# Performance work log

Hardware: AMD Instinct MI355X
Metric: run time of the kernel (lower is better)

Reference implementation:

```python
import jax, jax.numpy as jnp
import numpy as np

B, C, H, W = 8, 256, 64, 64
NH = 4
HD = C // NH
EPS_LN = 1e-5
EPS_NORM = 1e-12


def ln2d(x, w, b):
    # LayerNorm over channel dim of NCHW, per spatial location
    m = jnp.mean(x, axis=1, keepdims=True)
    v = jnp.mean((x - m) ** 2, axis=1, keepdims=True)
    return (x - m) / jnp.sqrt(v + EPS_LN) * w[None, :, None, None] + b[None, :, None, None]


def l2norm(x):
    # F.normalize(x, dim=-1)
    n = jnp.sqrt(jnp.sum(x * x, axis=-1, keepdims=True))
    return x / jnp.maximum(n, EPS_NORM)


def setup_inputs() -> dict:
    key = jax.random.key(0)
    ks = jax.random.split(key, 12)
    s = 0.02
    return {
        "img_feat": jax.random.normal(ks[0], (B, C, H, W), jnp.float32),
        "aux0": jax.random.normal(ks[1], (B, C, H, W), jnp.float32),
        "aux1": jax.random.normal(ks[2], (B, C, H, W), jnp.float32),
        "q_ln_w": jnp.ones((C,), jnp.float32),
        "q_ln_b": jnp.zeros((C,), jnp.float32),
        "kv_ln_w": jnp.ones((C,), jnp.float32),
        "kv_ln_b": jnp.zeros((C,), jnp.float32),
        "Wq": jax.random.normal(ks[3], (C, C), jnp.float32) * s,
        "Wkv": jax.random.normal(ks[4], (2 * C, C), jnp.float32) * s,
        "Wo": jax.random.normal(ks[5], (C, C), jnp.float32) * s,
        "bo": jnp.zeros((C,), jnp.float32),
        "attn_scale": jnp.zeros((NH, 1, 1), jnp.float32),
        "mlp_ln_w": jnp.ones((C,), jnp.float32),
        "mlp_ln_b": jnp.zeros((C,), jnp.float32),
        "W1": jax.random.normal(ks[6], (C, C), jnp.float32) * s,
        "b1": jnp.zeros((C,), jnp.float32),
        "W2": jax.random.normal(ks[7], (C, C), jnp.float32) * s,
        "b2": jnp.zeros((C,), jnp.float32),
    }


def reference(img_feat, aux0, aux1, q_ln_w, q_ln_b, kv_ln_w, kv_ln_b,
              Wq, Wkv, Wo, bo, attn_scale, mlp_ln_w, mlp_ln_b, W1, b1, W2, b2):
    HWn = H * W
    # q branch
    q = ln2d(img_feat, q_ln_w, q_ln_b).reshape(B, C, HWn)
    q = jnp.einsum('oc,bcn->bon', Wq, q).reshape(B, NH, HD, HWn)
    # kv branch: cat aux feats along batch (2B)
    kv_in = jnp.concatenate([aux0, aux1], axis=0)
    kv = ln2d(kv_in, kv_ln_w, kv_ln_b).reshape(2 * B, C, HWn)
    kv = jnp.einsum('oc,bcn->bon', Wkv, kv).reshape(2 * B, 2, NH, HD, HWn)
    k, v = kv[:, 0], kv[:, 1]  # each (2B, nh, hd, hw)
    qn = l2norm(q)
    kn = l2norm(k)
    kt, kd = kn[:B], kn[B:]
    vt, vd = v[:B], v[B:]
    # transposed (cross-covariance) cosine attention: hd x hd score matrix
    tex_attn = jax.nn.softmax(jnp.einsum('bnch,bndh->bncd', qn, kt), axis=-1)
    dep_attn = jax.nn.softmax(jnp.einsum('bnch,bndh->bncd', qn, kd), axis=-1)
    tex_qkv = jnp.einsum('bncd,bndh->bnch', tex_attn, vt)
    dep_qkv = jnp.einsum('bncd,bndh->bnch', dep_attn, vd)
    gate = jax.nn.sigmoid(attn_scale)[None]  # (1, nh, 1, 1)
    qkv = gate * tex_qkv + (1.0 - gate) * dep_qkv  # (B, nh, hd, hw)
    qkv = qkv.reshape(B, C, HWn)
    o = jnp.einsum('oc,bcn->bon', Wo, qkv).reshape(B, C, H, W) + bo[None, :, None, None]
    x = img_feat + o
    # ConvMlp (norm_ffn): LayerNorm2d -> 1x1 conv -> GELU -> 1x1 conv
    y = ln2d(x, mlp_ln_w, mlp_ln_b).reshape(B, C, HWn)
    y = jnp.einsum('oc,bcn->bon', W1, y) + b1[None, :, None]
    y = jax.nn.gelu(y)
    y = jnp.einsum('oc,bcn->bon', W2, y) + b2[None, :, None]
    return x + y.reshape(B, C, H, W)
```

## Files before the change

kernel.cpp:

```cpp
#include <hip/hip_runtime.h>
#include <math.h>
#include <stdint.h>

#define B_   8
#define C_   256
#define N_   4096

typedef __bf16 bf16;
typedef __bf16 bf16x8 __attribute__((ext_vector_type(8)));
typedef __bf16 bf16x4 __attribute__((ext_vector_type(4)));
typedef float  f32x4  __attribute__((ext_vector_type(4)));

#define MFMA16(a, b, c) __builtin_amdgcn_mfma_f32_16x16x32_bf16((a), (b), (c), 0, 0, 0)

struct Ptrs { const void* p[18]; };

__device__ __forceinline__ f32x4 ld4(const void* p, long i, bool f32) {
    f32x4 r;
    if (f32) {
        r = *(const f32x4*)((const float*)p + i);
    } else {
        bf16x4 v = *(const bf16x4*)((const bf16*)p + i);
        r[0] = (float)v[0]; r[1] = (float)v[1]; r[2] = (float)v[2]; r[3] = (float)v[3];
    }
    return r;
}

__device__ __forceinline__ float wave_sum(float s) {
    #pragma unroll
    for (int off = 32; off; off >>= 1) s += __shfl_xor(s, off);
    return s;
}

__device__ __forceinline__ void gl_lds16(const bf16* g, bf16* l) {
    __builtin_amdgcn_global_load_lds(
        (const __attribute__((address_space(1))) void*)(uintptr_t)g,
        (__attribute__((address_space(3))) void*)(uintptr_t)l, 16, 0, 0);
}

__global__ __launch_bounds__(256) void prep_kernel(Ptrs a, bf16* __restrict__ wb,
                                                   float* __restrict__ Sbuf,
                                                   bf16* __restrict__ biasb) {
    bool f32 = ((const unsigned*)a.p[3])[0] == 0x3F800000u;
    int row = blockIdx.x * 4 + (threadIdx.x >> 6);
    int lane = threadIdx.x & 63;
    long c4 = lane * 4;
    if (row >= 1536) {
        if (row == 1539) {
            if (lane == 0) {
                f32x4 v = ld4(a.p[11], 0, f32);
                #pragma unroll
                for (int j = 0; j < 4; ++j) biasb[768 + j] = (bf16)v[j];
            }
        } else {
            const void* s = (row == 1536) ? a.p[10] : (row == 1537) ? a.p[15] : a.p[17];
            f32x4 v = ld4(s, c4, f32);
            bf16x4 o;
            #pragma unroll
            for (int j = 0; j < 4; ++j) o[j] = (bf16)v[j];
            *(bf16x4*)(biasb + (row - 1536) * 256 + c4) = o;
        }
        return;
    }
    const void *W, *lw = nullptr, *lb = nullptr;
    long wrow; bf16* dst; float *s1 = nullptr, *s2 = nullptr;
    if (row < 256)       { W = a.p[7];  lw = a.p[3];  lb = a.p[4];  wrow = row;        dst = wb + row * 256;                 s1 = Sbuf + row;          s2 = Sbuf + 256 + row; }
    else if (row < 768)  { W = a.p[8];  lw = a.p[5];  lb = a.p[6];  wrow = row - 256;  dst = wb + 65536 + wrow * 256;        s1 = Sbuf + 512 + wrow;   s2 = Sbuf + 1024 + wrow; }
    else if (row < 1024) { W = a.p[14]; lw = a.p[12]; lb = a.p[13]; wrow = row - 768;  dst = wb + 196608 + wrow * 256;       s1 = Sbuf + 1536 + wrow;  s2 = Sbuf + 1792 + wrow; }
    else if (row < 1280) { W = a.p[9];  wrow = row - 1024; dst = wb + 262144 + wrow * 256; }
    else                 { W = a.p[16]; wrow = row - 1280; dst = wb + 327680 + wrow * 256; }
    f32x4 W4 = ld4(W, wrow * 256 + c4, f32);
    f32x4 w4, b4;
    if (lw) { w4 = ld4(lw, c4, f32); b4 = ld4(lb, c4, f32); }
    else    { w4[0]=w4[1]=w4[2]=w4[3]=1.f; b4[0]=b4[1]=b4[2]=b4[3]=0.f; }
    bf16x4 o;
    float s1v = 0.f, s2v = 0.f;
    #pragma unroll
    for (int j = 0; j < 4; ++j) {
        float wp = W4[j] * w4[j];
        o[j] = (bf16)wp;
        s1v += wp;
        s2v += W4[j] * b4[j];
    }
    *(bf16x4*)(dst + c4) = o;
    if (s1) {
        s1v = wave_sum(s1v); s2v = wave_sum(s2v);
        if (lane == 0) { *s1 = s1v; *s2 = s2v; }
    }
}

__global__ __launch_bounds__(256) void transpose_kernel(Ptrs a, bf16* __restrict__ xT) {
    bool f32 = ((const unsigned*)a.p[3])[0] == 0x3F800000u;
    int gt = blockIdx.z;
    const void* src; int batch;
    if (gt < 8)       { src = a.p[0]; batch = gt; }
    else if (gt < 16) { src = a.p[1]; batch = gt - 8; }
    else              { src = a.p[2]; batch = gt - 16; }
    int c0 = blockIdx.y * 64, n0 = blockIdx.x * 64;
    int t = threadIdx.x;
    __shared__ bf16 T[64][72];
    int cl = t >> 4, n4 = (t & 15) * 4;
    #pragma unroll
    for (int i = 0; i < 4; ++i) {
        int c = i * 16 + cl;
        f32x4 v = ld4(src, ((long)batch * 256 + c0 + c) * 4096 + n0 + n4, f32);
        #pragma unroll
        for (int j = 0; j < 4; ++j) T[c][n4 + j] = (bf16)v[j];
    }
    __syncthreads();
    int c8 = (t & 7) * 8, nl = t >> 3;
    #pragma unroll
    for (int j = 0; j < 2; ++j) {
        int n = j * 32 + nl;
        bf16x8 o;
        #pragma unroll
        for (int jj = 0; jj < 8; ++jj) o[jj] = T[c8 + jj][n];
        *(bf16x8*)(xT + ((size_t)gt * 4096 + n0 + n) * 256 + c0 + c8) = o;
    }
}

__global__ __launch_bounds__(256) void statsT_kernel(const bf16* __restrict__ xT,
                                                     float2* __restrict__ st) {
    int row = blockIdx.x * 4 + (threadIdx.x >> 6);
    int lane = threadIdx.x & 63;
    bf16x4 v = *(const bf16x4*)(xT + (size_t)row * 256 + lane * 4);
    float s = 0.f, q = 0.f;
    #pragma unroll
    for (int j = 0; j < 4; ++j) { float f = (float)v[j]; s += f; q += f * f; }
    s = wave_sum(s); q = wave_sum(q);
    if (lane == 0) {
        float mean = s * (1.0f / 256.0f);
        float var  = q * (1.0f / 256.0f) - mean * mean;
        float2 o; o.x = mean; o.y = rsqrtf(var + 1e-5f);
        st[row] = o;
    }
}

__global__ __launch_bounds__(256, 2) void wgemm_kernel(const bf16* __restrict__ A,
                                                    const bf16* __restrict__ xT,
                                                    const float2* __restrict__ stats,
                                                    const float* __restrict__ S1,
                                                    const float* __restrict__ S2,
                                                    const bf16* __restrict__ bias,
                                                    const bf16* __restrict__ resT,
                                                    void* __restrict__ out,
                                                    bf16* __restrict__ vT,
                                                    const unsigned* __restrict__ probe,
                                                    int emode, int gelu) {
    int n0 = blockIdx.x * 128;
    int ot = blockIdx.y;
    int g  = blockIdx.z;
    int t = threadIdx.x, wv = t >> 6, lane = t & 63;
    int m16 = lane & 15, quad = lane >> 4;
    int wr = wv >> 1, wc = wv & 1;
    int rl = lane >> 3, slot = lane & 7;

    __shared__ bf16 As[2][128 * 64];
    __shared__ bf16 Bs[2][128 * 64];

    const bf16* Agbase = A + (size_t)ot * 128 * 256;
    const bf16* Bgbase = xT + ((size_t)g * 4096 + n0) * 256;

    auto stage = [&](int buf, int ks) {
        #pragma unroll
        for (int i = 0; i < 4; ++i) {
            int row = wv * 32 + i * 8 + rl;
            int koff = ks * 64 + ((slot ^ (row & 7)) << 3);
            bf16* ldsA = &As[buf][(wv * 32 + i * 8) * 64];
            bf16* ldsB = &Bs[buf][(wv * 32 + i * 8) * 64];
            gl_lds16(Agbase + (size_t)row * 256 + koff, ldsA);
            gl_lds16(Bgbase + (size_t)row * 256 + koff, ldsB);
        }
    };

    f32x4 acc[4][4];
    #pragma unroll
    for (int i = 0; i < 4; ++i)
        #pragma unroll
        for (int j = 0; j < 4; ++j) acc[i][j] = (f32x4){0.f, 0.f, 0.f, 0.f};

    auto compute = [&](int buf) {
        #pragma unroll
        for (int kf = 0; kf < 2; ++kf) {
            bf16x8 af[4], bv[4];
            #pragma unroll
            for (int mt = 0; mt < 4; ++mt) {
                int r = wr * 64 + mt * 16 + m16;
                af[mt] = *(const bf16x8*)&As[buf][r * 64 + (((kf * 4 + quad) ^ (r & 7)) << 3)];
            }
            #pragma unroll
            for (int nt = 0; nt < 4; ++nt) {
                int r = wc * 64 + nt * 16 + m16;
                bv[nt] = *(const bf16x8*)&Bs[buf][r * 64 + (((kf * 4 + quad) ^ (r & 7)) << 3)];
            }
            #pragma unroll
            for (int mt = 0; mt < 4; ++mt)
                #pragma unroll
                for (int nt = 0; nt < 4; ++nt)
                    acc[mt][nt] = MFMA16(af[mt], bv[nt], acc[mt][nt]);
        }
    };

    stage(0, 0);
    __syncthreads();
    #pragma unroll
    for (int ks = 0; ks < 4; ++ks) {
        if (ks < 3) stage((ks + 1) & 1, ks + 1);
        compute(ks & 1);
        __syncthreads();
    }

    int of32 = (emode == 3) ? (probe[0] == 0x3F800000u) : 0;

    #pragma unroll
    for (int mt = 0; mt < 4; ++mt) {
        int olb  = wr * 64 + mt * 16 + quad * 4;
        int orow = ot * 128 + olb;
        f32x4 s1v, s2v, bz;
        if (stats) { s1v = *(const f32x4*)(S1 + orow); s2v = *(const f32x4*)(S2 + orow); }
        if (bias) {
            bf16x4 bb = *(const bf16x4*)(bias + orow);
            #pragma unroll
            for (int r = 0; r < 4; ++r) bz[r] = (float)bb[r];
        }
        #pragma unroll
        for (int nt = 0; nt < 4; ++nt) {
            int n = n0 + wc * 64 + nt * 16 + m16;
            f32x4 v = acc[mt][nt];
            if (stats) {
                float2 st = stats[(size_t)g * N_ + n];
                float a1 = st.y, a2 = -st.y * st.x;
                #pragma unroll
                for (int r = 0; r < 4; ++r) v[r] = a1 * v[r] + a2 * s1v[r] + s2v[r];
            }
            if (bias) {
                #pragma unroll
                for (int r = 0; r < 4; ++r) v[r] += bz[r];
            }
            if (gelu) {
                #pragma unroll
                for (int r = 0; r < 4; ++r) {
                    float x = v[r];
                    float u = x + 0.044715f * x * x * x;
                    v[r] = 0.5f * x * (1.0f + tanhf(0.7978845608028654f * u));
                }
            }
            if (emode == 0) {
                if (vT == nullptr || orow < 256) {
                    bf16* o = (bf16*)out;
                    #pragma unroll
                    for (int r = 0; r < 4; ++r)
                        o[((size_t)(g * 256 + orow + r)) * N_ + n] = (bf16)v[r];
                } else {
                    int od = orow - 256;
                    int hh = od >> 6, d0 = od & 63;
                    bf16x4 tmp;
                    #pragma unroll
                    for (int r = 0; r < 4; ++r) tmp[r] = (bf16)v[r];
                    *(bf16x4*)(vT + (((size_t)(g * 4 + hh)) * N_ + n) * 64 + d0) = tmp;
                }
            } else if (emode == 2) {
                size_t idx = ((size_t)g * N_ + n) * 256 + orow;
                if (resT) {
                    bf16x4 rr = *(const bf16x4*)(resT + idx);
                    #pragma unroll
                    for (int r = 0; r < 4; ++r) v[r] += (float)rr[r];
                }
                bf16x4 tmp;
                #pragma unroll
                for (int r = 0; r < 4; ++r) tmp[r] = (bf16)v[r];
                *(bf16x4*)((bf16*)out + idx) = tmp;
            } else {
                bf16x4 rr = *(const bf16x4*)(resT + ((size_t)g * N_ + n) * 256 + orow);
                #pragma unroll
                for (int r = 0; r < 4; ++r) {
                    float val = v[r] + (float)rr[r];
                    size_t oi = ((size_t)(g * 256 + orow + r)) * N_ + n;
                    if (of32) ((float*)out)[oi] = val;
                    else      ((bf16*)out)[oi] = (bf16)val;
                }
            }
        }
    }
}

__global__ __launch_bounds__(256) void rownorm_kernel(const bf16* __restrict__ x,
                                                      float* __restrict__ invn) {
    size_t row = blockIdx.x;
    const bf16* p = x + (row << 12);
    int t = threadIdx.x;
    float s = 0.f;
    #pragma unroll
    for (int i = 0; i < 2; ++i) {
        bf16x8 v = *(const bf16x8*)(p + ((size_t)(i * 256 + t) << 3));
        #pragma unroll
        for (int j = 0; j < 8; ++j) { float f = (float)v[j]; s += f * f; }
    }
    #pragma unroll
    for (int off = 32; off > 0; off >>= 1) s += __shfl_down(s, off);
    __shared__ float ps[4];
    if ((t & 63) == 0) ps[t >> 6] = s;
    __syncthreads();
    if (t == 0) {
        float tot = ps[0] + ps[1] + ps[2] + ps[3];
        invn[row] = 1.0f / fmaxf(sqrtf(tot), 1e-12f);
    }
}

__global__ __launch_bounds__(256) void sgemm_kernel(const bf16* __restrict__ q,
                                                    const bf16* __restrict__ k,
                                                    float* __restrict__ Spart) {
    int bh = blockIdx.x, ks = blockIdx.y;
    int b = bh >> 2, h = bh & 3;
    int t = threadIdx.x, wv = t >> 6, lane = t & 63;
    int m16 = lane & 15, quad = lane >> 4;
    const bf16* qrow = q + (size_t)(b * 256 + h * 64 + wv * 16 + m16) * N_;
    const bf16* kt0  = k + (size_t)(b * 256 + h * 64) * N_;
    const bf16* kd0  = k + (size_t)((b + 8) * 256 + h * 64) * N_;

    f32x4 at[4], ad[4];
    #pragma unroll
    for (int i = 0; i < 4; ++i) { at[i] = (f32x4){0.f,0.f,0.f,0.f}; ad[i] = (f32x4){0.f,0.f,0.f,0.f}; }

    int nbeg = ks * 512;
    for (int n = nbeg; n < nbeg + 512; n += 32) {
        int ko = n + quad * 8;
        bf16x8 a = *(const bf16x8*)(qrow + ko);
        #pragma unroll
        for (int dt = 0; dt < 4; ++dt) {
            bf16x8 bt = *(const bf16x8*)(kt0 + (size_t)(dt * 16 + m16) * N_ + ko);
            at[dt] = MFMA16(a, bt, at[dt]);
            bf16x8 bd = *(const bf16x8*)(kd0 + (size_t)(dt * 16 + m16) * N_ + ko);
            ad[dt] = MFMA16(a, bd, ad[dt]);
        }
    }
    float* oT = Spart + (size_t)(ks * 32 + bh) * 4096;
    float* oD = Spart + (size_t)8 * 32 * 4096 + (size_t)(ks * 32 + bh) * 4096;
    #pragma unroll
    for (int dt = 0; dt < 4; ++dt)
        #pragma unroll
        for (int r = 0; r < 4; ++r) {
            int c = wv * 16 + quad * 4 + r, d = dt * 16 + m16;
            oT[c * 64 + d] = at[dt][r];
            oD[c * 64 + d] = ad[dt][r];
        }
}

__global__ __launch_bounds__(256) void softmax_kernel(const float* __restrict__ Spart,
                                                      const float* __restrict__ invnq,
                                                      const float* __restrict__ invnk,
                                                      const bf16* __restrict__ attn_scale,
                                                      bf16* __restrict__ Acat) {
    int bh = blockIdx.x;
    int h = bh & 3;
    int t = threadIdx.x, wv = t >> 6, lane = t & 63;
    float g = 1.0f / (1.0f + expf(-(float)attn_scale[h]));
    #pragma unroll
    for (int i = 0; i < 4; ++i) {
        int idx = blockIdx.y * 16 + wv * 4 + i;
        int stream = idx >> 6, c = idx & 63;
        const float* Sp = Spart + (size_t)stream * 8 * 32 * 4096 + (size_t)bh * 4096 + c * 64 + lane;
        float s = 0.f;
        #pragma unroll
        for (int ks = 0; ks < 8; ++ks) s += Sp[(size_t)ks * 32 * 4096];
        s *= invnq[bh * 64 + c] * invnk[(stream ? bh + 32 : bh) * 64 + lane];
        float mx = s;
        #pragma unroll
        for (int off = 32; off > 0; off >>= 1) mx = fmaxf(mx, __shfl_xor(mx, off));
        float e = expf(s - mx);
        float sum = e;
        #pragma unroll
        for (int off = 32; off > 0; off >>= 1) sum += __shfl_xor(sum, off);
        float a = e / sum * (stream == 0 ? g : 1.0f - g);
        Acat[(size_t)bh * 8192 + c * 128 + stream * 64 + lane] = (bf16)a;
    }
}

__global__ __launch_bounds__(256) void av_kernel(const bf16* __restrict__ Acat,
                                                 const bf16* __restrict__ vT,
                                                 bf16* __restrict__ qkvT) {
    int pt = blockIdx.x, h = blockIdx.y, b = blockIdx.z;
    int bh = b * 4 + h;
    int t = threadIdx.x, wv = t >> 6, lane = t & 63;
    int m16 = lane & 15, quad = lane >> 4;
    int p0 = pt * 64;

    const bf16* Arow = Acat + (size_t)bh * 8192 + (size_t)(wv * 16 + m16) * 128 + quad * 8;
    bf16x8 a[4];
    #pragma unroll
    for (int ds = 0; ds < 4; ++ds) a[ds] = *(const bf16x8*)(Arow + ds * 32);

    f32x4 acc[4];
    #pragma unroll
    for (int i = 0; i < 4; ++i) acc[i] = (f32x4){0.f,0.f,0.f,0.f};

    #pragma unroll
    for (int nt = 0; nt < 4; ++nt) {
        int p = p0 + nt * 16 + m16;
        #pragma unroll
        for (int ds = 0; ds < 4; ++ds) {
            int stream = ds >> 1;
            int dl = (ds & 1) * 32 + quad * 8;
            const bf16* vb = vT + (((size_t)(b + 8 * stream) * 4 + h) * N_ + p) * 64 + dl;
            bf16x8 bv = *(const bf16x8*)vb;
            acc[nt] = MFMA16(a[ds], bv, acc[nt]);
        }
    }
    #pragma unroll
    for (int nt = 0; nt < 4; ++nt) {
        int p = p0 + nt * 16 + m16;
        int cbase = h * 64 + wv * 16 + quad * 4;
        bf16x4 o;
        #pragma unroll
        for (int r = 0; r < 4; ++r) o[r] = (bf16)acc[nt][r];
        *(bf16x4*)(qkvT + ((size_t)b * 4096 + p) * 256 + cbase) = o;
    }
}

extern "C" void kernel_launch(void* const* d_in, const int* in_sizes, int n_in,
                              void* d_out, int out_size, void* d_ws, size_t ws_size,
                              hipStream_t stream) {
    (void)in_sizes; (void)n_in; (void)out_size; (void)ws_size;

    Ptrs args;
    for (int i = 0; i < 18; ++i) args.p[i] = d_in[i];
    const unsigned* probe = (const unsigned*)d_in[3];

    char* ws = (char*)d_ws;
    size_t off = 0;
    auto alloc = [&](size_t bytes) { char* p = ws + off; off += (bytes + 255) & ~(size_t)255; return p; };
    bf16*   xTall = (bf16*)alloc(50331648);
    float2* stAll = (float2*)alloc(786432);
    float2* stX   = (float2*)alloc(262144);
    bf16*   wb    = (bf16*)alloc(786432);
    float*  Sbuf  = (float*)alloc(8192);
    bf16*   biasb = (bf16*)alloc(2048);
    bf16*   q     = (bf16*)alloc(16777216);
    bf16*   k     = (bf16*)alloc(33554432);
    bf16*   vT    = (bf16*)alloc(33554432);
    float*  Spart = (float*)alloc(8388608);
    bf16*   Acat  = (bf16*)alloc(524288);
    float*  invnq = (float*)alloc(8192);
    float*  invnk = (float*)alloc(16384);

    bf16* imgT  = xTall;
    bf16* auxT  = xTall + (size_t)8 * 4096 * 256;
    bf16* qkvT  = q;
    bf16* xbufT = k;
    bf16* h1T   = auxT;

    prep_kernel<<<385, 256, 0, stream>>>(args, wb, Sbuf, biasb);
    transpose_kernel<<<dim3(64, 4, 24), 256, 0, stream>>>(args, xTall);
    statsT_kernel<<<24576, 256, 0, stream>>>(xTall, stAll);
    wgemm_kernel<<<dim3(32, 2, 8),  256, 0, stream>>>(wb,         imgT, stAll,            Sbuf,       Sbuf + 256,  nullptr, nullptr, q, nullptr, probe, 0, 0);
    wgemm_kernel<<<dim3(32, 4, 16), 256, 0, stream>>>(wb + 65536, auxT, stAll + 8 * 4096, Sbuf + 512, Sbuf + 1024, nullptr, nullptr, k, vT,      probe, 0, 0);
    rownorm_kernel<<<2048, 256, 0, stream>>>(q, invnq);
    rownorm_kernel<<<4096, 256, 0, stream>>>(k, invnk);
    sgemm_kernel<<<dim3(32, 8), 256, 0, stream>>>(q, k, Spart);
    softmax_kernel<<<dim3(32, 8), 256, 0, stream>>>(Spart, invnq, invnk, biasb + 768, Acat);
    av_kernel<<<dim3(64, 4, 8), 256, 0, stream>>>(Acat, vT, qkvT);
    wgemm_kernel<<<dim3(32, 2, 8), 256, 0, stream>>>(wb + 262144, qkvT, nullptr, nullptr, nullptr, biasb, imgT, xbufT, nullptr, probe, 2, 0);
    statsT_kernel<<<8192, 256, 0, stream>>>(xbufT, stX);
    wgemm_kernel<<<dim3(32, 2, 8), 256, 0, stream>>>(wb + 196608, xbufT, stX, Sbuf + 1536, Sbuf + 1792, biasb + 256, nullptr, h1T, nullptr, probe, 2, 1);
    wgemm_kernel<<<dim3(32, 2, 8), 256, 0, stream>>>(wb + 327680, h1T, nullptr, nullptr, nullptr, biasb + 512, xbufT, d_out, nullptr, probe, 3, 0);
}
```

Before: 388.4 us.

## Fuse LayerNorm stats into transpose and single-buffer GEMM LDS for occupancy

```diff
diff --git a/kernel.cpp b/kernel.cpp
--- a/kernel.cpp
+++ b/kernel.cpp
@@ -89,33 +89,53 @@
     }
 }
 
-__global__ __launch_bounds__(256) void transpose_kernel(Ptrs a, bf16* __restrict__ xT) {
+__global__ __launch_bounds__(256) void transpose_kernel(Ptrs a, bf16* __restrict__ xT,
+                                                        float2* __restrict__ st) {
     bool f32 = ((const unsigned*)a.p[3])[0] == 0x3F800000u;
     int gt = blockIdx.z;
     const void* src; int batch;
     if (gt < 8)       { src = a.p[0]; batch = gt; }
     else if (gt < 16) { src = a.p[1]; batch = gt - 8; }
     else              { src = a.p[2]; batch = gt - 16; }
-    int c0 = blockIdx.y * 64, n0 = blockIdx.x * 64;
+    int n0 = blockIdx.x * 64;
     int t = threadIdx.x;
     __shared__ bf16 T[64][72];
     int cl = t >> 4, n4 = (t & 15) * 4;
-    #pragma unroll
-    for (int i = 0; i < 4; ++i) {
-        int c = i * 16 + cl;
-        f32x4 v = ld4(src, ((long)batch * 256 + c0 + c) * 4096 + n0 + n4, f32);
-        #pragma unroll
-        for (int j = 0; j < 4; ++j) T[c][n4 + j] = (bf16)v[j];
-    }
-    __syncthreads();
     int c8 = (t & 7) * 8, nl = t >> 3;
+    float sa[2] = {0.f, 0.f}, qa[2] = {0.f, 0.f};
+    for (int ct = 0; ct < 4; ++ct) {
+        int c0 = ct * 64;
+        if (ct) __syncthreads();
+        #pragma unroll
+        for (int i = 0; i < 4; ++i) {
+            int c = i * 16 + cl;
+            f32x4 v = ld4(src, ((long)batch * 256 + c0 + c) * 4096 + n0 + n4, f32);
+            #pragma unroll
+            for (int j = 0; j < 4; ++j) T[c][n4 + j] = (bf16)v[j];
+        }
+        __syncthreads();
+        #pragma unroll
+        for (int j = 0; j < 2; ++j) {
+            int n = j * 32 + nl;
+            bf16x8 o;
+            #pragma unroll
+            for (int jj = 0; jj < 8; ++jj) o[jj] = T[c8 + jj][n];
+            *(bf16x8*)(xT + ((size_t)gt * 4096 + n0 + n) * 256 + c0 + c8) = o;
+            #pragma unroll
+            for (int jj = 0; jj < 8; ++jj) { float f = (float)o[jj]; sa[j] += f; qa[j] += f * f; }
+        }
+    }
     #pragma unroll
     for (int j = 0; j < 2; ++j) {
-        int n = j * 32 + nl;
-        bf16x8 o;
-        #pragma unroll
-        for (int jj = 0; jj < 8; ++jj) o[jj] = T[c8 + jj][n];
-        *(bf16x8*)(xT + ((size_t)gt * 4096 + n0 + n) * 256 + c0 + c8) = o;
+        float s = sa[j], q = qa[j];
+        #pragma unroll
+        for (int off = 1; off < 8; off <<= 1) { s += __shfl_xor(s, off); q += __shfl_xor(q, off); }
+        if ((t & 7) == 0) {
+            float mean = s * (1.0f / 256.0f);
+            float var  = q * (1.0f / 256.0f) - mean * mean;
+            float2 o2; o2.x = mean; o2.y = rsqrtf(var + 1e-5f);
+            st[(size_t)gt * 4096 + n0 + j * 32 + nl] = o2;
+        }
     }
 }
 
@@ -136,7 +156,7 @@
     }
 }
 
-__global__ __launch_bounds__(256, 2) void wgemm_kernel(const bf16* __restrict__ A,
+__global__ __launch_bounds__(256, 4) void wgemm_kernel(const bf16* __restrict__ A,
                                                     const bf16* __restrict__ xT,
                                                     const float2* __restrict__ stats,
                                                     const float* __restrict__ S1,
@@ -155,21 +175,19 @@
     int wr = wv >> 1, wc = wv & 1;
     int rl = lane >> 3, slot = lane & 7;
 
-    __shared__ bf16 As[2][128 * 64];
-    __shared__ bf16 Bs[2][128 * 64];
+    __shared__ bf16 As[128 * 64];
+    __shared__ bf16 Bs[128 * 64];
 
     const bf16* Agbase = A + (size_t)ot * 128 * 256;
     const bf16* Bgbase = xT + ((size_t)g * 4096 + n0) * 256;
 
-    auto stage = [&](int buf, int ks) {
+    auto stage = [&](int ks) {
         #pragma unroll
         for (int i = 0; i < 4; ++i) {
             int row = wv * 32 + i * 8 + rl;
             int koff = ks * 64 + ((slot ^ (row & 7)) << 3);
-            bf16* ldsA = &As[buf][(wv * 32 + i * 8) * 64];
-            bf16* ldsB = &Bs[buf][(wv * 32 + i * 8) * 64];
-            gl_lds16(Agbase + (size_t)row * 256 + koff, ldsA);
-            gl_lds16(Bgbase + (size_t)row * 256 + koff, ldsB);
+            gl_lds16(Agbase + (size_t)row * 256 + koff, &As[(wv * 32 + i * 8) * 64]);
+            gl_lds16(Bgbase + (size_t)row * 256 + koff, &Bs[(wv * 32 + i * 8) * 64]);
         }
     };
 
@@ -179,19 +197,19 @@
         #pragma unroll
         for (int j = 0; j < 4; ++j) acc[i][j] = (f32x4){0.f, 0.f, 0.f, 0.f};
 
-    auto compute = [&](int buf) {
+    auto compute = [&]() {
         #pragma unroll
         for (int kf = 0; kf < 2; ++kf) {
             bf16x8 af[4], bv[4];
             #pragma unroll
             for (int mt = 0; mt < 4; ++mt) {
                 int r = wr * 64 + mt * 16 + m16;
-                af[mt] = *(const bf16x8*)&As[buf][r * 64 + (((kf * 4 + quad) ^ (r & 7)) << 3)];
+                af[mt] = *(const bf16x8*)&As[r * 64 + (((kf * 4 + quad) ^ (r & 7)) << 3)];
             }
             #pragma unroll
             for (int nt = 0; nt < 4; ++nt) {
                 int r = wc * 64 + nt * 16 + m16;
-                bv[nt] = *(const bf16x8*)&Bs[buf][r * 64 + (((kf * 4 + quad) ^ (r & 7)) << 3)];
+                bv[nt] = *(const bf16x8*)&Bs[r * 64 + (((kf * 4 + quad) ^ (r & 7)) << 3)];
             }
             #pragma unroll
             for (int mt = 0; mt < 4; ++mt)
@@ -201,13 +219,12 @@
         }
     };
 
-    stage(0, 0);
-    __syncthreads();
     #pragma unroll
     for (int ks = 0; ks < 4; ++ks) {
-        if (ks < 3) stage((ks + 1) & 1, ks + 1);
-        compute(ks & 1);
+        if (ks) __syncthreads();
+        stage(ks);
         __syncthreads();
+        compute();
     }
 
     int of32 = (emode == 3) ? (probe[0] == 0x3F800000u) : 0;
@@ -450,8 +467,7 @@
     bf16* h1T   = auxT;
 
     prep_kernel<<<385, 256, 0, stream>>>(args, wb, Sbuf, biasb);
-    transpose_kernel<<<dim3(64, 4, 24), 256, 0, stream>>>(args, xTall);
-    statsT_kernel<<<24576, 256, 0, stream>>>(xTall, stAll);
+    transpose_kernel<<<dim3(64, 1, 24), 256, 0, stream>>>(args, xTall, stAll);
     wgemm_kernel<<<dim3(32, 2, 8),  256, 0, stream>>>(wb,         imgT, stAll,            Sbuf,       Sbuf + 256,  nullptr, nullptr, q, nullptr, probe, 0, 0);
     wgemm_kernel<<<dim3(32, 4, 16), 256, 0, stream>>>(wb + 65536, auxT, stAll + 8 * 4096, Sbuf + 512, Sbuf + 1024, nullptr, nullptr, k, vT,      probe, 0, 0);
     rownorm_kernel<<<2048, 256, 0, stream>>>(q, invnq);
```

Result: no change. 383.7 us (-1.2%).
